# Kernel optimization log

Measured on AMD Instinct MI355X. Metric: run time of the kernel, lower is better.

The kernel has to match this reference:

```python
import jax, jax.numpy as jnp
import numpy as np

N_HEAD = 16
NEG = -1e9

def setup_inputs() -> dict:
    key = jax.random.key(0)
    k1, k2, k3 = jax.random.split(key, 3)
    B, S, NX = 8, 1024, 1024
    x = jax.random.normal(k1, (B, S, NX), dtype=jnp.float32)
    w_attn = jax.random.normal(k2, (NX, 3 * NX), dtype=jnp.float32) * 0.02
    b_attn = jnp.zeros((3 * NX,), dtype=jnp.float32)
    w_proj = jax.random.normal(k3, (NX, NX), dtype=jnp.float32) * 0.02
    b_proj = jnp.zeros((NX,), dtype=jnp.float32)
    return {"x": x, "w_attn": w_attn, "b_attn": b_attn, "w_proj": w_proj, "b_proj": b_proj}

def reference(x, w_attn, b_attn, w_proj, b_proj):
    B, S, NX = x.shape
    H = N_HEAD
    D = NX // H
    qkv = x @ w_attn + b_attn                      # [B,S,3*NX]
    q, k, v = jnp.split(qkv, 3, axis=-1)           # each [B,S,NX]
    q = q.reshape(B, S, H, D)
    k = k.reshape(B, S, H, D)
    v = v.reshape(B, S, H, D)
    # scores with scale (scale=True -> divide by sqrt(head_dim))
    w = jnp.einsum('bqhd,bkhd->bhqk', q, k) / jnp.sqrt(jnp.float32(D))
    tril = jnp.tril(jnp.ones((S, S), dtype=w.dtype))  # causal mask buffer
    w = w * tril + NEG * (1.0 - tril)
    w = jax.nn.softmax(w, axis=-1)                 # dropout is identity at eval
    a = jnp.einsum('bhqk,bkhd->bqhd', w, v)        # [B,S,H,D]
    a = a.reshape(B, S, NX)
    a = a @ w_proj + b_proj
    return a
```

## Files before the change

### kernel.cpp

```cpp
#include <hip/hip_runtime.h>
#include <hip/hip_bf16.h>
#include <stdint.h>

typedef __bf16 bf16x8 __attribute__((ext_vector_type(8)));
typedef float  f32x4  __attribute__((ext_vector_type(4)));
typedef float  f32x16 __attribute__((ext_vector_type(16)));

#define BARRIER() asm volatile("s_barrier" ::: "memory")
#define VMCNT(n)  asm volatile("s_waitcnt vmcnt(" #n ")" ::: "memory")
#define LGKM0()   asm volatile("s_waitcnt lgkmcnt(0)" ::: "memory")
#define SCHED0()  __builtin_amdgcn_sched_barrier(0)

__device__ __forceinline__ void gload_lds16(const void* g, void* l) {
  __builtin_amdgcn_global_load_lds(
      (const __attribute__((address_space(1))) unsigned int*)g,
      (__attribute__((address_space(3))) unsigned int*)l, 16, 0, 0);
}

__global__ void k_cast(const float* __restrict__ in, __bf16* __restrict__ out, int n4) {
  int i = blockIdx.x * blockDim.x + threadIdx.x;
  if (i >= n4) return;
  float4 v = reinterpret_cast<const float4*>(in)[i];
  union { __bf16 h[4]; uint64_t u; } c;
  c.h[0] = (__bf16)v.x; c.h[1] = (__bf16)v.y; c.h[2] = (__bf16)v.z; c.h[3] = (__bf16)v.w;
  *reinterpret_cast<uint64_t*>(out + 4l * i) = c.u;
}

__global__ void k_transpose_cast(const float* __restrict__ in, __bf16* __restrict__ out,
                                 int R, int C) {
  __shared__ float t[32][33];
  const int tx = threadIdx.x & 31, ty = threadIdx.x >> 5;
  const int c0 = blockIdx.x * 32, r0 = blockIdx.y * 32;
#pragma unroll
  for (int rr = 0; rr < 4; ++rr)
    t[ty * 4 + rr][tx] = in[(long)(r0 + ty * 4 + rr) * C + c0 + tx];
  __syncthreads();
#pragma unroll
  for (int rr = 0; rr < 4; ++rr)
    out[(long)(c0 + ty * 4 + rr) * R + r0 + tx] = (__bf16)t[tx][ty * 4 + rr];
}

template <int MODE>
__launch_bounds__(512, 2)
__global__ void k_gemm_p(const __bf16* __restrict__ A, const __bf16* __restrict__ Bt,
                         const float* __restrict__ bias, int M, int N, int K, int NB,
                         __bf16* __restrict__ qo, __bf16* __restrict__ ko,
                         __bf16* __restrict__ vo, float* __restrict__ fo) {
  __shared__ __bf16 lds[3][24576];
  const int tid = threadIdx.x;
  const int l = tid & 63;
  const int w = tid >> 6;
  const int lm = l & 15, lq = l >> 4;
  const int wm = w >> 2, wn = w & 3;
  const int nwg = gridDim.x;
  const int wg = (blockIdx.x & 7) * (nwg >> 3) + (blockIdx.x >> 3);
  const int bm = wg / NB, bn = wg % NB;
  const int nt = K >> 6;

  const int rA = tid >> 3;
  const int scol = (((tid & 7) * 16) ^ ((rA & 7) << 4)) >> 1;
  long a_off[4], b_off[2];
#pragma unroll
  for (int li = 0; li < 4; ++li) a_off[li] = (long)(bm * 256 + li * 64 + rA) * K + scol;
#pragma unroll
  for (int li = 0; li < 2; ++li) b_off[li] = (long)(bn * 128 + li * 64 + rA) * K + scol;

#define STAGE_A(buf, t) { \
    gload_lds16(A + a_off[0] + (long)(t) * 64, &lds[buf][tid * 8]); \
    gload_lds16(A + a_off[1] + (long)(t) * 64, &lds[buf][4096 + tid * 8]); \
    gload_lds16(A + a_off[2] + (long)(t) * 64, &lds[buf][8192 + tid * 8]); \
    gload_lds16(A + a_off[3] + (long)(t) * 64, &lds[buf][12288 + tid * 8]); }
#define STAGE_B(buf, t) { \
    gload_lds16(Bt + b_off[0] + (long)(t) * 64, &lds[buf][16384 + tid * 8]); \
    gload_lds16(Bt + b_off[1] + (long)(t) * 64, &lds[buf][20480 + tid * 8]); }

  const int aswz = (lm & 7) << 4;
  const int cofs0 = ((0 * 64 + lq * 16) ^ aswz) >> 1;
  const int cofs1 = ((1 * 64 + lq * 16) ^ aswz) >> 1;
  const int arow = wm * 128 + lm;
  const int brow = wn * 32 + lm;

  f32x4 acc[8][2] = {};

  STAGE_A(0, 0); STAGE_B(0, 0);
  STAGE_A(1, 1); STAGE_B(1, 1);
  VMCNT(6); BARRIER();

  for (int t = 0; t < nt; ++t) {
    const int cb = t % 3;
    const __bf16* Lb = lds[cb];
    bf16x8 bf[2][2], af[4][2];
#pragma unroll
    for (int nj = 0; nj < 2; ++nj) {
      bf[nj][0] = *(const bf16x8*)&Lb[16384 + (brow + nj * 16) * 64 + cofs0];
      bf[nj][1] = *(const bf16x8*)&Lb[16384 + (brow + nj * 16) * 64 + cofs1];
    }
#pragma unroll
    for (int mi = 0; mi < 4; ++mi) {
      af[mi][0] = *(const bf16x8*)&Lb[(arow + mi * 16) * 64 + cofs0];
      af[mi][1] = *(const bf16x8*)&Lb[(arow + mi * 16) * 64 + cofs1];
    }
    if (t + 2 < nt) STAGE_A((t + 2) % 3, t + 2);
    BARRIER();
    LGKM0(); SCHED0();
    __builtin_amdgcn_s_setprio(1);
#pragma unroll
    for (int ks = 0; ks < 2; ++ks)
#pragma unroll
      for (int mi = 0; mi < 4; ++mi)
#pragma unroll
        for (int nj = 0; nj < 2; ++nj)
          acc[mi][nj] = __builtin_amdgcn_mfma_f32_16x16x32_bf16(af[mi][ks], bf[nj][ks],
                                                                acc[mi][nj], 0, 0, 0);
    __builtin_amdgcn_s_setprio(0);
    SCHED0();
    BARRIER();
#pragma unroll
    for (int mi = 0; mi < 4; ++mi) {
      af[mi][0] = *(const bf16x8*)&Lb[(arow + (mi + 4) * 16) * 64 + cofs0];
      af[mi][1] = *(const bf16x8*)&Lb[(arow + (mi + 4) * 16) * 64 + cofs1];
    }
    if (t + 2 < nt) {
      STAGE_B((t + 2) % 3, t + 2);
      VMCNT(6);
    } else {
      VMCNT(0);
    }
    BARRIER();
    LGKM0(); SCHED0();
    __builtin_amdgcn_s_setprio(1);
#pragma unroll
    for (int ks = 0; ks < 2; ++ks)
#pragma unroll
      for (int mi = 0; mi < 4; ++mi)
#pragma unroll
        for (int nj = 0; nj < 2; ++nj)
          acc[mi + 4][nj] = __builtin_amdgcn_mfma_f32_16x16x32_bf16(af[mi][ks], bf[nj][ks],
                                                                    acc[mi + 4][nj], 0, 0, 0);
    __builtin_amdgcn_s_setprio(0);
    SCHED0();
    BARRIER();
  }

  if (MODE == 0) {
#pragma unroll
    for (int nj = 0; nj < 2; ++nj) {
      const int c = bn * 128 + wn * 32 + nj * 16 + lm;
      const float bv = bias[c];
      const int which = c >> 10, cc = c & 1023, hh = cc >> 6, d = cc & 63;
#pragma unroll
      for (int mi = 0; mi < 8; ++mi)
#pragma unroll
        for (int i = 0; i < 4; ++i) {
          const int r = bm * 256 + wm * 128 + mi * 16 + lq * 4 + i;
          const int b = r >> 10, s_ = r & 1023;
          float fv = acc[mi][nj][i] + bv;
          if (which == 0) fv *= 0.125f;
          const __bf16 v = (__bf16)fv;
          const long hb = (long)(b * 16 + hh);
          if (which == 0)      qo[(hb * 1024 + s_) * 64 + d] = v;
          else if (which == 1) ko[(hb * 1024 + s_) * 64 + d] = v;
          else                 vo[(hb * 64 + d) * 1024 + s_] = v;
        }
    }
  } else {
#pragma unroll
    for (int nj = 0; nj < 2; ++nj) {
      const int c = bn * 128 + wn * 32 + nj * 16 + lm;
      const float bv = bias[c];
#pragma unroll
      for (int mi = 0; mi < 8; ++mi)
#pragma unroll
        for (int i = 0; i < 4; ++i) {
          const int r = bm * 256 + wm * 128 + mi * 16 + lq * 4 + i;
          fo[(long)r * N + c] = acc[mi][nj][i] + bv;
        }
    }
  }
#undef STAGE_A
#undef STAGE_B
}

__device__ __forceinline__ void attn_qtile(const __bf16* __restrict__ Q,
                                           const __bf16* __restrict__ Kh,
                                           const __bf16* __restrict__ Vt,
                                           __bf16* __restrict__ ob,
                                           int b, int h, int qbw, int l) {
  const int lm = l & 31, hi = l >> 5;

  bf16x8 qf[4];
#pragma unroll
  for (int ds = 0; ds < 4; ++ds)
    qf[ds] = *(const bf16x8*)(Q + (long)(qbw + lm) * 64 + ds * 16 + hi * 8);

  f32x16 oacc0 = {}, oacc1 = {};
  float m = -__builtin_inff(), s = 0.f;

  const int ntiles = (qbw >> 5) + 1;
  for (int kt = 0; kt < ntiles; ++kt) {
    const int k0 = kt * 32;
    f32x16 st = {};
#pragma unroll
    for (int ds = 0; ds < 4; ++ds) {
      bf16x8 kf = *(const bf16x8*)(Kh + (long)(k0 + lm) * 64 + ds * 16 + hi * 8);
      st = __builtin_amdgcn_mfma_f32_32x32x16_bf16(kf, qf[ds], st, 0, 0, 0);
    }
    if (kt == ntiles - 1) {
      const int q = qbw + lm;
#pragma unroll
      for (int r = 0; r < 16; ++r) {
        const int key = k0 + (r & 3) + 8 * (r >> 2) + 4 * hi;
        if (key > q) st[r] = -__builtin_inff();
      }
    }
    float tm = st[0];
#pragma unroll
    for (int r = 1; r < 16; ++r) tm = fmaxf(tm, st[r]);
    tm = fmaxf(tm, __shfl_xor(tm, 32));
    if (!__all(tm <= m + 8.f)) {
      const float mn = fmaxf(m, tm);
      const float fac = __expf(m - mn);
      m = mn;
      s *= fac;
#pragma unroll
      for (int r = 0; r < 16; ++r) {
        const int qr = (r & 3) + 8 * (r >> 2) + 4 * hi;
        const float fr = __int_as_float(
            __builtin_amdgcn_ds_bpermute(qr * 4, __float_as_int(fac)));
        oacc0[r] *= fr; oacc1[r] *= fr;
      }
    }
    float p[16], ts = 0.f;
#pragma unroll
    for (int r = 0; r < 16; ++r) { p[r] = __expf(st[r] - m); ts += p[r]; }
    ts += __shfl_xor(ts, 32);
    s += ts;
    unsigned int w8[8];
#pragma unroll
    for (int t = 0; t < 8; ++t) {
      union { __bf16 hh[2]; unsigned int u; } pk;
      pk.hh[0] = (__bf16)p[2 * t]; pk.hh[1] = (__bf16)p[2 * t + 1];
      w8[t] = pk.u;
    }
    const unsigned int e0 = __shfl_xor(hi ? w8[0] : w8[2], 32);
    const unsigned int e1 = __shfl_xor(hi ? w8[1] : w8[3], 32);
    const unsigned int e2 = __shfl_xor(hi ? w8[4] : w8[6], 32);
    const unsigned int e3 = __shfl_xor(hi ? w8[5] : w8[7], 32);
    union { unsigned int wd[4]; bf16x8 v; } pa0, pa1;
    if (hi) {
      pa0.wd[0] = e0;    pa0.wd[1] = e1;    pa0.wd[2] = w8[2]; pa0.wd[3] = w8[3];
      pa1.wd[0] = e2;    pa1.wd[1] = e3;    pa1.wd[2] = w8[6]; pa1.wd[3] = w8[7];
    } else {
      pa0.wd[0] = w8[0]; pa0.wd[1] = w8[1]; pa0.wd[2] = e0;    pa0.wd[3] = e1;
      pa1.wd[0] = w8[4]; pa1.wd[1] = w8[5]; pa1.wd[2] = e2;    pa1.wd[3] = e3;
    }
#pragma unroll
    for (int t = 0; t < 2; ++t) {
      const bf16x8 pa = t ? pa1.v : pa0.v;
      bf16x8 vf0 = *(const bf16x8*)(Vt + (long)lm * 1024 + k0 + t * 16 + hi * 8);
      bf16x8 vf1 = *(const bf16x8*)(Vt + (long)(32 + lm) * 1024 + k0 + t * 16 + hi * 8);
      oacc0 = __builtin_amdgcn_mfma_f32_32x32x16_bf16(pa, vf0, oacc0, 0, 0, 0);
      oacc1 = __builtin_amdgcn_mfma_f32_32x32x16_bf16(pa, vf1, oacc1, 0, 0, 0);
    }
  }
  const float invs = 1.f / s;
#pragma unroll
  for (int r = 0; r < 16; ++r) {
    const int qr = (r & 3) + 8 * (r >> 2) + 4 * hi;
    const float inv = __int_as_float(
        __builtin_amdgcn_ds_bpermute(qr * 4, __float_as_int(invs)));
    const long row = (long)(b * 1024 + qbw + qr) * 1024 + h * 64;
    ob[row + lm]      = (__bf16)(oacc0[r] * inv);
    ob[row + 32 + lm] = (__bf16)(oacc1[r] * inv);
  }
}

__global__ void k_attn(const __bf16* __restrict__ qb_, const __bf16* __restrict__ kb,
                       const __bf16* __restrict__ vtb, __bf16* __restrict__ ob) {
  const int l = threadIdx.x & 63, w = threadIdx.x >> 6;
  const int bid = blockIdx.x;
  const int xcd = bid & 7, slot = bid >> 3;
  const int bh = xcd + 8 * (slot >> 2);
  const int j = slot & 3;
  const int wi = j * 4 + w;
  const int b = bh >> 4, h = bh & 15;
  const __bf16* Q  = qb_ + (long)bh * 65536;
  const __bf16* Kh = kb  + (long)bh * 65536;
  const __bf16* Vt = vtb + (long)bh * 65536;
  attn_qtile(Q, Kh, Vt, ob, b, h, wi * 32, l);
  attn_qtile(Q, Kh, Vt, ob, b, h, (31 - wi) * 32, l);
}

extern "C" void kernel_launch(void* const* d_in, const int* in_sizes, int n_in,
                              void* d_out, int out_size, void* d_ws, size_t ws_size,
                              hipStream_t stream) {
  const float* x      = (const float*)d_in[0];
  const float* w_attn = (const float*)d_in[1];
  const float* b_attn = (const float*)d_in[2];
  const float* w_proj = (const float*)d_in[3];
  const float* b_proj = (const float*)d_in[4];
  float* out = (float*)d_out;

  char* ws = (char*)d_ws;
  const size_t SZ_XBF = (size_t)8192 * 1024 * 2;
  __bf16* x_bf = (__bf16*)ws;  ws += SZ_XBF;
  __bf16* wat  = (__bf16*)ws;  ws += (size_t)3072 * 1024 * 2;
  __bf16* wpt  = (__bf16*)ws;  ws += (size_t)1024 * 1024 * 2;
  __bf16* qb   = (__bf16*)ws;  ws += SZ_XBF;
  __bf16* kb   = (__bf16*)ws;  ws += SZ_XBF;
  __bf16* vtb  = (__bf16*)ws;  ws += SZ_XBF;
  __bf16* obf  = (__bf16*)ws;  ws += SZ_XBF;

  k_cast<<<8192, 256, 0, stream>>>(x, x_bf, 2097152);
  k_transpose_cast<<<dim3(96, 32), 256, 0, stream>>>(w_attn, wat, 1024, 3072);
  k_transpose_cast<<<dim3(32, 32), 256, 0, stream>>>(w_proj, wpt, 1024, 1024);
  k_gemm_p<0><<<768, 512, 0, stream>>>(x_bf, wat, b_attn, 8192, 3072, 1024, 24,
                                       qb, kb, vtb, nullptr);
  k_attn<<<512, 256, 0, stream>>>(qb, kb, vtb, obf);
  k_gemm_p<1><<<256, 512, 0, stream>>>(obf, wpt, b_proj, 8192, 1024, 1024, 8,
                                       nullptr, nullptr, nullptr, out);
}
```

Measured before the change: 287.5 us.

## Split GEMM k-tile into four phases with finer-grained LDS prefetch interleave

Restructures the GEMM main loop from two compute phases per 64-wide k-tile into four, splitting along both the M halves and the two k-substeps. The global-to-LDS prefetch is spread across three phases (A rows 0-1, A rows 2-3, B) so each phase issues fewer loads. This also halves the fragment registers held per phase. The cost is twice as many barriers per tile. The vmcnt wait is also changed so it is skipped on the final iteration.

```diff
diff --git a/kernel.cpp b/kernel.cpp
--- a/kernel.cpp
+++ b/kernel.cpp
@@ -65,12 +65,13 @@
 #pragma unroll
   for (int li = 0; li < 2; ++li) b_off[li] = (long)(bn * 128 + li * 64 + rA) * K + scol;
 
-#define STAGE_A(buf, t) { \
+#define STAGE_A01(buf, t) { \
     gload_lds16(A + a_off[0] + (long)(t) * 64, &lds[buf][tid * 8]); \
-    gload_lds16(A + a_off[1] + (long)(t) * 64, &lds[buf][4096 + tid * 8]); \
+    gload_lds16(A + a_off[1] + (long)(t) * 64, &lds[buf][4096 + tid * 8]); }
+#define STAGE_A23(buf, t) { \
     gload_lds16(A + a_off[2] + (long)(t) * 64, &lds[buf][8192 + tid * 8]); \
     gload_lds16(A + a_off[3] + (long)(t) * 64, &lds[buf][12288 + tid * 8]); }
-#define STAGE_B(buf, t) { \
+#define STAGE_B01(buf, t) { \
     gload_lds16(Bt + b_off[0] + (long)(t) * 64, &lds[buf][16384 + tid * 8]); \
     gload_lds16(Bt + b_off[1] + (long)(t) * 64, &lds[buf][20480 + tid * 8]); }
 
@@ -82,64 +83,76 @@
 
   f32x4 acc[8][2] = {};
 
-  STAGE_A(0, 0); STAGE_B(0, 0);
-  STAGE_A(1, 1); STAGE_B(1, 1);
+  STAGE_A01(0, 0); STAGE_A23(0, 0); STAGE_B01(0, 0);
+  STAGE_A01(1, 1); STAGE_A23(1, 1); STAGE_B01(1, 1);
   VMCNT(6); BARRIER();
 
   for (int t = 0; t < nt; ++t) {
-    const int cb = t % 3;
-    const __bf16* Lb = lds[cb];
-    bf16x8 bf[2][2], af[4][2];
-#pragma unroll
-    for (int nj = 0; nj < 2; ++nj) {
-      bf[nj][0] = *(const bf16x8*)&Lb[16384 + (brow + nj * 16) * 64 + cofs0];
-      bf[nj][1] = *(const bf16x8*)&Lb[16384 + (brow + nj * 16) * 64 + cofs1];
-    }
-#pragma unroll
-    for (int mi = 0; mi < 4; ++mi) {
-      af[mi][0] = *(const bf16x8*)&Lb[(arow + mi * 16) * 64 + cofs0];
-      af[mi][1] = *(const bf16x8*)&Lb[(arow + mi * 16) * 64 + cofs1];
-    }
-    if (t + 2 < nt) STAGE_A((t + 2) % 3, t + 2);
-    BARRIER();
-    LGKM0(); SCHED0();
+    const __bf16* Lb = lds[t % 3];
+    const int sb = (t + 2) % 3;
+    const bool st = (t + 2 < nt);
+    bf16x8 bf[2], af[4];
+
+    bf[0] = *(const bf16x8*)&Lb[16384 + (brow) * 64 + cofs0];
+    bf[1] = *(const bf16x8*)&Lb[16384 + (brow + 16) * 64 + cofs0];
+#pragma unroll
+    for (int j = 0; j < 4; ++j)
+      af[j] = *(const bf16x8*)&Lb[(arow + j * 16) * 64 + cofs0];
+    if (st) STAGE_A01(sb, t + 2);
+    BARRIER(); LGKM0(); SCHED0();
     __builtin_amdgcn_s_setprio(1);
 #pragma unroll
-    for (int ks = 0; ks < 2; ++ks)
-#pragma unroll
-      for (int mi = 0; mi < 4; ++mi)
-#pragma unroll
-        for (int nj = 0; nj < 2; ++nj)
-          acc[mi][nj] = __builtin_amdgcn_mfma_f32_16x16x32_bf16(af[mi][ks], bf[nj][ks],
-                                                                acc[mi][nj], 0, 0, 0);
+    for (int j = 0; j < 4; ++j)
+#pragma unroll
+      for (int nj = 0; nj < 2; ++nj)
+        acc[j][nj] = __builtin_amdgcn_mfma_f32_16x16x32_bf16(af[j], bf[nj], acc[j][nj], 0, 0, 0);
     __builtin_amdgcn_s_setprio(0);
-    SCHED0();
-    BARRIER();
-#pragma unroll
-    for (int mi = 0; mi < 4; ++mi) {
-      af[mi][0] = *(const bf16x8*)&Lb[(arow + (mi + 4) * 16) * 64 + cofs0];
-      af[mi][1] = *(const bf16x8*)&Lb[(arow + (mi + 4) * 16) * 64 + cofs1];
-    }
-    if (t + 2 < nt) {
-      STAGE_B((t + 2) % 3, t + 2);
-      VMCNT(6);
-    } else {
-      VMCNT(0);
-    }
-    BARRIER();
-    LGKM0(); SCHED0();
+    SCHED0(); BARRIER();
+
+#pragma unroll
+    for (int j = 0; j < 4; ++j)
+      af[j] = *(const bf16x8*)&Lb[(arow + (j + 4) * 16) * 64 + cofs0];
+    if (st) STAGE_A23(sb, t + 2);
+    BARRIER(); LGKM0(); SCHED0();
     __builtin_amdgcn_s_setprio(1);
 #pragma unroll
-    for (int ks = 0; ks < 2; ++ks)
-#pragma unroll
-      for (int mi = 0; mi < 4; ++mi)
-#pragma unroll
-        for (int nj = 0; nj < 2; ++nj)
-          acc[mi + 4][nj] = __builtin_amdgcn_mfma_f32_16x16x32_bf16(af[mi][ks], bf[nj][ks],
-                                                                    acc[mi + 4][nj], 0, 0, 0);
+    for (int j = 0; j < 4; ++j)
+#pragma unroll
+      for (int nj = 0; nj < 2; ++nj)
+        acc[j + 4][nj] = __builtin_amdgcn_mfma_f32_16x16x32_bf16(af[j], bf[nj], acc[j + 4][nj], 0, 0, 0);
     __builtin_amdgcn_s_setprio(0);
-    SCHED0();
-    BARRIER();
+    SCHED0(); BARRIER();
+
+    bf[0] = *(const bf16x8*)&Lb[16384 + (brow) * 64 + cofs1];
+    bf[1] = *(const bf16x8*)&Lb[16384 + (brow + 16) * 64 + cofs1];
+#pragma unroll
+    for (int j = 0; j < 4; ++j)
+      af[j] = *(const bf16x8*)&Lb[(arow + j * 16) * 64 + cofs1];
+    if (st) STAGE_B01(sb, t + 2);
+    BARRIER(); LGKM0(); SCHED0();
+    __builtin_amdgcn_s_setprio(1);
+#pragma unroll
+    for (int j = 0; j < 4; ++j)
+#pragma unroll
+      for (int nj = 0; nj < 2; ++nj)
+        acc[j][nj] = __builtin_amdgcn_mfma_f32_16x16x32_bf16(af[j], bf[nj], acc[j][nj], 0, 0, 0);
+    __builtin_amdgcn_s_setprio(0);
+    SCHED0(); BARRIER();
+
+#pragma unroll
+    for (int j = 0; j < 4; ++j)
+      af[j] = *(const bf16x8*)&Lb[(arow + (j + 4) * 16) * 64 + cofs1];
+    if (st) { VMCNT(6); }
+    else if (t + 1 < nt) { VMCNT(0); }
+    BARRIER(); LGKM0(); SCHED0();
+    __builtin_amdgcn_s_setprio(1);
+#pragma unroll
+    for (int j = 0; j < 4; ++j)
+#pragma unroll
+      for (int nj = 0; nj < 2; ++nj)
+        acc[j + 4][nj] = __builtin_amdgcn_mfma_f32_16x16x32_bf16(af[j], bf[nj], acc[j + 4][nj], 0, 0, 0);
+    __builtin_amdgcn_s_setprio(0);
+    SCHED0(); BARRIER();
   }
 
   if (MODE == 0) {
@@ -177,8 +190,9 @@
         }
     }
   }
-#undef STAGE_A
-#undef STAGE_B
+#undef STAGE_A01
+#undef STAGE_A23
+#undef STAGE_B01
 }
 
 __device__ __forceinline__ void attn_qtile(const __bf16* __restrict__ Q,
```

Result: slower. 293.6 us (+2.1%).
